# Optimization experiments

Hardware: AMD Instinct MI355X
Metric: run time of the kernel (lower is better)

Reference implementation:

```python
import jax, jax.numpy as jnp
import numpy as np

B = 16384
DIM_IN = 128; DIM_OUT = 128; DIM_X = 512; DIM_NL = 128
EPS = 1e-3; ALPHA = 1.0; STD = 0.5
DIM_H = 2 * DIM_X + DIM_NL


def setup_inputs() -> dict:
    key = jax.random.key(0)
    ks = jax.random.split(key, 8)
    u_in = jax.random.normal(ks[0], (B, 1, DIM_IN), jnp.float32)
    X = STD * jax.random.normal(ks[1], (DIM_H, DIM_H), jnp.float32)
    Y = STD * jax.random.normal(ks[2], (DIM_X, DIM_X), jnp.float32)
    B2 = STD * jax.random.normal(ks[3], (DIM_X, DIM_IN), jnp.float32)
    C2 = STD * jax.random.normal(ks[4], (DIM_OUT, DIM_X), jnp.float32)
    D21 = STD * jax.random.normal(ks[5], (DIM_OUT, DIM_NL), jnp.float32)
    D22 = STD * jax.random.normal(ks[6], (DIM_OUT, DIM_IN), jnp.float32)
    D12 = STD * jax.random.normal(ks[7], (DIM_NL, DIM_IN), jnp.float32)
    x0 = jnp.zeros((1, 1, DIM_X), jnp.float32)
    return {"u_in": u_in, "X": X, "Y": Y, "B2": B2, "C2": C2,
            "D21": D21, "D22": D22, "D12": D12, "x0": x0}


def reference(u_in, X, Y, B2, C2, D21, D22, D12, x0):
    # --- derived contractive parameterization (torch _update_model_param) ---
    H = X.T @ X + EPS * jnp.eye(DIM_H, dtype=X.dtype)
    H11 = H[:DIM_X, :DIM_X]
    H21 = H[DIM_X:DIM_X + DIM_NL, :DIM_X]
    H22 = H[DIM_X:DIM_X + DIM_NL, DIM_X:DIM_X + DIM_NL]
    H31 = H[DIM_X + DIM_NL:, :DIM_X]
    H32 = H[DIM_X + DIM_NL:, DIM_X:DIM_X + DIM_NL]
    H33 = H[DIM_X + DIM_NL:, DIM_X + DIM_NL:]
    F = H31                               # [X, X]
    B1 = H32                              # [X, NL]
    E = 0.5 * (H11 + ALPHA * H33 + Y - Y.T)  # [X, X]
    Lam = 0.5 * jnp.diagonal(H22)            # [NL]
    D11 = -jnp.tril(H22, k=-1)               # strictly lower triangular [NL, NL]
    C1 = -H21                                # [NL, X]

    u = u_in[:, 0, :]      # [B, in]
    x = x0[0, 0, :]        # [X], broadcast over batch as in torch
    xc = C1 @ x            # [NL] (x @ C1row^T per row, shared across batch)
    ud = u @ D12.T         # [B, NL] (precomputed; same math as per-row matmul)

    # sequential forward-substitution with tanh per row (strict lower tri D11)
    def step(w, inp):
        i, d11row, xci, lam = inp
        v = xci + ud[:, i] + w @ d11row        # [B]
        return w.at[:, i].set(jnp.tanh(v / lam)), None

    w0 = jnp.zeros((u.shape[0], DIM_NL), u.dtype)
    w, _ = jax.lax.scan(step, w0, (jnp.arange(DIM_NL), D11, xc, Lam))

    # state update: x+ = (x F^T + w B1^T + u B2^T) E^{-T}
    pre = (F @ x)[None, :] + w @ B1.T + u @ B2.T   # [B, X]
    x_new = pre @ jnp.linalg.inv(E).T              # [B, X]
    # output
    y = x_new @ C2.T + w @ D21.T + u @ D22.T       # [B, out]
    return y[:, None, :]
```

## Files before the change

### kernel.cpp

```cpp
#include <hip/hip_runtime.h>
#include <math.h>

#define EPS_C 0.001f
#define BATCH 16384

__global__ __launch_bounds__(256) void k_xtx(const float* __restrict__ X, float* __restrict__ H) {
  __shared__ float smem[64 * 65];
  const int bi64 = blockIdx.x, bj64 = blockIdx.y;
  if (bi64 > bj64) return;
  float (*sA)[65] = (float(*)[65])smem;
  float (*sB)[65] = (float(*)[65])(smem + 32 * 65);
  const int t = threadIdx.x;
  const int bi = bi64 * 64, bj = bj64 * 64;
  const int tj = t & 15, ti = t >> 4;
  float acc[4][4] = {};
  for (int k0 = 0; k0 < 1152; k0 += 32) {
    #pragma unroll
    for (int l = 0; l < 2; ++l) {
      int idx = t + l * 256;
      int kk = idx >> 4, c4 = (idx & 15) << 2;
      float4 va = *(const float4*)&X[(k0 + kk) * 1152 + bi + c4];
      sA[kk][c4 + 0] = va.x; sA[kk][c4 + 1] = va.y; sA[kk][c4 + 2] = va.z; sA[kk][c4 + 3] = va.w;
      float4 vb = *(const float4*)&X[(k0 + kk) * 1152 + bj + c4];
      sB[kk][c4 + 0] = vb.x; sB[kk][c4 + 1] = vb.y; sB[kk][c4 + 2] = vb.z; sB[kk][c4 + 3] = vb.w;
    }
    __syncthreads();
    #pragma unroll
    for (int kk = 0; kk < 32; ++kk) {
      float am[4], bn[4];
      #pragma unroll
      for (int q = 0; q < 4; ++q) am[q] = sA[kk][ti * 4 + q];
      #pragma unroll
      for (int q = 0; q < 4; ++q) bn[q] = sB[kk][tj * 4 + q];
      #pragma unroll
      for (int r = 0; r < 4; ++r)
        #pragma unroll
        for (int c = 0; c < 4; ++c)
          acc[r][c] = fmaf(am[r], bn[c], acc[r][c]);
    }
    __syncthreads();
  }
  #pragma unroll
  for (int r = 0; r < 4; ++r) {
    int gi = bi + ti * 4 + r;
    float vv[4];
    #pragma unroll
    for (int c = 0; c < 4; ++c) {
      vv[c] = acc[r][c];
      if (gi == bj + tj * 4 + c) vv[c] += EPS_C;
    }
    float4 o = make_float4(vv[0], vv[1], vv[2], vv[3]);
    *(float4*)&H[gi * 1152 + bj + tj * 4] = o;
  }
  if (bi64 < bj64) {
    float (*tr)[65] = (float(*)[65])smem;
    #pragma unroll
    for (int r = 0; r < 4; ++r)
      #pragma unroll
      for (int c = 0; c < 4; ++c)
        tr[tj * 4 + c][ti * 4 + r] = acc[r][c];
    __syncthreads();
    #pragma unroll
    for (int l = 0; l < 4; ++l) {
      int e = t + l * 256;
      int row = e >> 4, c4 = (e & 15) << 2;
      float4 o = make_float4(tr[row][c4], tr[row][c4 + 1], tr[row][c4 + 2], tr[row][c4 + 3]);
      *(float4*)&H[(bj + row) * 1152 + bi + c4] = o;
    }
  }
}

__global__ __launch_bounds__(256) void k_assemble(const float* __restrict__ H, const float* __restrict__ Y,
                           const float* __restrict__ C2, const float* __restrict__ x0,
                           float* __restrict__ M, float* __restrict__ D11,
                           float* __restrict__ Lam, float* __restrict__ xc, float* __restrict__ Fx) {
  const int b = blockIdx.x;
  const int t = threadIdx.x;
  if (b < 256) {
    __shared__ float tA[32][33], tB[32][33], tC[32][33];
    const int R0 = (b & 15) * 32, C0 = (b >> 4) * 32;
    const int c = t & 31, rr = t >> 5;
    #pragma unroll
    for (int p = 0; p < 4; ++p) {
      int row = rr + p * 8;
      tA[row][c] = H[(C0 + row) * 1152 + R0 + c];
      tB[row][c] = H[(640 + C0 + row) * 1152 + 640 + R0 + c];
      tC[row][c] = Y[(C0 + row) * 512 + R0 + c];
    }
    __syncthreads();
    #pragma unroll
    for (int p = 0; p < 4; ++p) {
      int r = rr + p * 8;
      float val = 0.5f * (tA[c][r] + tB[c][r] + tC[c][r] - Y[(R0 + r) * 512 + C0 + c]);
      M[(R0 + r) * 640 + C0 + c] = val;
    }
  } else if (b < 320) {
    int e0 = (b - 256) * 1024;
    #pragma unroll
    for (int l = 0; l < 4; ++l) {
      int e = e0 + l * 256 + t;
      int r = e >> 7, o = e & 127;
      M[r * 640 + 512 + o] = C2[o * 512 + r];
    }
  } else if (b < 384) {
    int e = (b - 320) * 256 + t;
    int i = e >> 7, j = e & 127;
    D11[e] = (j < i) ? -H[(512 + i) * 1152 + 512 + j] : 0.0f;
  } else if (b == 384) {
    if (t < 128) Lam[t] = 0.5f * H[(512 + t) * 1152 + 512 + t];
  } else if (b == 385) {
    if (t < 128) {
      float s = 0.f;
      for (int a = 0; a < 512; ++a) s = fmaf(H[(512 + t) * 1152 + a], x0[a], s);
      xc[t] = -s;
    }
  } else {
    int r = (b - 386) * 256 + t;
    float s = 0.f;
    for (int a = 0; a < 512; ++a) s = fmaf(H[(640 + r) * 1152 + a], x0[a], s);
    Fx[r] = s;
  }
}

__global__ __launch_bounds__(64) void k_lu_dp(float* __restrict__ M, float* __restrict__ Dfac, int kb) {
  __shared__ float sD[64 * 65];
  __shared__ float sRD[64];
  const int t = threadIdx.x;
  const int nU = 9 - kb;
  const int pb = blockIdx.x;
  float v[64];
  int c = 0, rr = 0;
  if (pb < nU) {
    c = 64 * (kb + 1) + pb * 64 + t;
    #pragma unroll
    for (int i = 0; i < 64; ++i) v[i] = M[(kb * 64 + i) * 640 + c];
  } else {
    rr = 64 * (kb + 1) + (pb - nU) * 64 + t;
    #pragma unroll
    for (int i = 0; i < 16; ++i) *(float4*)&v[i * 4] = *(const float4*)&M[rr * 640 + kb * 64 + i * 4];
  }
  {
    const float* blk = M + kb * 64 * 640 + kb * 64;
    float col[64];
    #pragma unroll
    for (int r = 0; r < 64; ++r) col[r] = blk[r * 640 + t];
    float invp = 1.0f;
    #pragma unroll
    for (int k = 0; k < 64; ++k) {
      float piv = __shfl(col[k], k);
      float inv = 1.0f / piv;
      if (t == k) invp = inv;
      float m = col[k] * inv;
      bool act = t > k;
      #pragma unroll
      for (int r = k + 1; r < 64; ++r) {
        float ckr = __shfl(col[r], k);
        if (act) col[r] -= ckr * m;
      }
    }
    #pragma unroll
    for (int r = 0; r < 64; ++r) {
      if (r > t) col[r] *= invp;
      sD[r * 65 + t] = col[r];
      if (pb == 0) Dfac[kb * 4096 + r * 64 + t] = col[r];
    }
    sRD[t] = invp;
  }
  __syncthreads();
  if (pb < nU) {
    #pragma unroll
    for (int i = 1; i < 64; ++i) {
      float a0 = v[i], a1 = 0.f;
      #pragma unroll
      for (int j = 0; j < i; j += 2) {
        a0 = fmaf(-sD[i * 65 + j], v[j], a0);
        if (j + 1 < i) a1 = fmaf(-sD[i * 65 + j + 1], v[j + 1], a1);
      }
      v[i] = a0 + a1;
    }
    #pragma unroll
    for (int i = 0; i < 64; ++i) M[(kb * 64 + i) * 640 + c] = v[i];
  } else {
    #pragma unroll
    for (int j = 0; j < 64; ++j) {
      float a0 = v[j], a1 = 0.f;
      #pragma unroll
      for (int i = 0; i < j; i += 2) {
        a0 = fmaf(-v[i], sD[i * 65 + j], a0);
        if (i + 1 < j) a1 = fmaf(-v[i + 1], sD[(i + 1) * 65 + j], a1);
      }
      v[j] = (a0 + a1) * sRD[j];
    }
    #pragma unroll
    for (int i = 0; i < 16; ++i) *(float4*)&M[rr * 640 + kb * 64 + i * 4] = *(float4*)&v[i * 4];
  }
}

__global__ __launch_bounds__(256) void k_lu_trailing(float* __restrict__ M, int kb) {
  __shared__ float sL[32][65];
  __shared__ float sU[32][65];
  const int t = threadIdx.x;
  const int base = 64 * (kb + 1);
  const int r0 = base + blockIdx.y * 64, c0 = base + blockIdx.x * 64;
  const int tj = t & 15, ti = t >> 4;
  float acc[4][4] = {};
  for (int k0 = 0; k0 < 64; k0 += 32) {
    #pragma unroll
    for (int l = 0; l < 2; ++l) {
      int idx = t + l * 256;
      int row = idx >> 3, k4 = (idx & 7) << 2;
      float4 v = *(const float4*)&M[(r0 + row) * 640 + kb * 64 + k0 + k4];
      sL[k4 + 0][row] = v.x; sL[k4 + 1][row] = v.y; sL[k4 + 2][row] = v.z; sL[k4 + 3][row] = v.w;
      int kk = idx >> 4, c4 = (idx & 15) << 2;
      float4 u4 = *(const float4*)&M[(kb * 64 + k0 + kk) * 640 + c0 + c4];
      sU[kk][c4 + 0] = u4.x; sU[kk][c4 + 1] = u4.y; sU[kk][c4 + 2] = u4.z; sU[kk][c4 + 3] = u4.w;
    }
    __syncthreads();
    #pragma unroll
    for (int kk = 0; kk < 32; ++kk) {
      float am[4], bn[4];
      #pragma unroll
      for (int q = 0; q < 4; ++q) am[q] = sL[kk][ti * 4 + q];
      #pragma unroll
      for (int q = 0; q < 4; ++q) bn[q] = sU[kk][tj * 4 + q];
      #pragma unroll
      for (int r = 0; r < 4; ++r)
        #pragma unroll
        for (int c = 0; c < 4; ++c)
          acc[r][c] = fmaf(am[r], bn[c], acc[r][c]);
    }
    __syncthreads();
  }
  #pragma unroll
  for (int r = 0; r < 4; ++r) {
    float4 old = *(float4*)&M[(r0 + ti * 4 + r) * 640 + c0 + tj * 4];
    old.x -= acc[r][0]; old.y -= acc[r][1]; old.z -= acc[r][2]; old.w -= acc[r][3];
    *(float4*)&M[(r0 + ti * 4 + r) * 640 + c0 + tj * 4] = old;
  }
}

__global__ __launch_bounds__(64) void k_inv(const float* __restrict__ Dfac, float* __restrict__ invU) {
  __shared__ float sD[64 * 65];
  __shared__ float srs[64];
  const int t = threadIdx.x;
  const int kb = blockIdx.x;
  for (int l = 0; l < 64; ++l) sD[l * 65 + t] = Dfac[kb * 4096 + l * 64 + t];
  __syncthreads();
  srs[t] = 1.0f / sD[t * 65 + t];
  __syncthreads();
  float v[64];
  #pragma unroll
  for (int i = 0; i < 64; ++i) v[i] = (i == t) ? srs[t] : 0.0f;
  #pragma unroll
  for (int i = 62; i >= 0; --i) {
    float a0 = 0.f, a1 = 0.f;
    #pragma unroll
    for (int j = i + 1; j < 64; j += 2) {
      a0 = fmaf(-sD[i * 65 + j], v[j], a0);
      if (j + 1 < 64) a1 = fmaf(-sD[i * 65 + j + 1], v[j + 1], a1);
    }
    float nv = (a0 + a1) * srs[i];
    v[i] = (i == t) ? v[i] : nv;
  }
  #pragma unroll
  for (int i = 0; i < 64; ++i) invU[kb * 4096 + i * 64 + t] = v[i];
}

__global__ __launch_bounds__(512, 2) void k_bs(const float* __restrict__ M, const float* __restrict__ invUg,
                                               float* __restrict__ Gt) {
  __shared__ float sZ[512 * 17];
  __shared__ float sU[64 * 65];
  __shared__ float sI[64 * 65];
  const int t = threadIdx.x;
  const int c0 = blockIdx.x * 16;
  const int o = t & 15, q = t >> 4;
  #pragma unroll
  for (int l = 0; l < 16; ++l) {
    int e = t + l * 512;
    int r = e >> 4, oo = e & 15;
    sZ[r * 17 + oo] = M[r * 640 + 512 + c0 + oo];
  }
  for (int kb = 7; kb >= 0; --kb) {
    #pragma unroll
    for (int l = 0; l < 8; ++l) {
      int e = t + l * 512;
      int r = e >> 6, k = e & 63;
      sI[r * 65 + k] = invUg[kb * 4096 + r * 64 + k];
    }
    __syncthreads();
    float xv[2];
    #pragma unroll
    for (int rr = 0; rr < 2; ++rr) {
      int i = q * 2 + rr;
      float a0 = 0.f, a1 = 0.f;
      #pragma unroll
      for (int k = 0; k < 64; k += 2) {
        a0 = fmaf(sI[i * 65 + k], sZ[(kb * 64 + k) * 17 + o], a0);
        a1 = fmaf(sI[i * 65 + k + 1], sZ[(kb * 64 + k + 1) * 17 + o], a1);
      }
      xv[rr] = a0 + a1;
    }
    __syncthreads();
    #pragma unroll
    for (int rr = 0; rr < 2; ++rr) {
      int i = q * 2 + rr;
      sZ[(kb * 64 + i) * 17 + o] = xv[rr];
      Gt[(kb * 64 + i) * 128 + c0 + o] = xv[rr];
    }
    __syncthreads();
    if (kb == 0) break;
    float xk[64];
    #pragma unroll
    for (int k = 0; k < 64; ++k) xk[k] = sZ[(kb * 64 + k) * 17 + o];
    float bufA[8], bufB[8];
    #pragma unroll
    for (int l = 0; l < 8; ++l) {
      int e = t + l * 512;
      int r = e >> 6, k = e & 63;
      bufA[l] = M[r * 640 + kb * 64 + k];
    }
    for (int i = 0; i < kb; ++i) {
      #pragma unroll
      for (int l = 0; l < 8; ++l) {
        int e = t + l * 512;
        int r = e >> 6, k = e & 63;
        sU[r * 65 + k] = bufA[l];
      }
      if (i + 1 < kb) {
        #pragma unroll
        for (int l = 0; l < 8; ++l) {
          int e = t + l * 512;
          int r = e >> 6, k = e & 63;
          bufB[l] = M[((i + 1) * 64 + r) * 640 + kb * 64 + k];
        }
      }
      __syncthreads();
      #pragma unroll
      for (int rr = 0; rr < 2; ++rr) {
        int row = q * 2 + rr;
        float acc = sZ[(i * 64 + row) * 17 + o];
        #pragma unroll
        for (int k = 0; k < 64; ++k)
          acc = fmaf(-sU[row * 65 + k], xk[k], acc);
        sZ[(i * 64 + row) * 17 + o] = acc;
      }
      #pragma unroll
      for (int l = 0; l < 8; ++l) bufA[l] = bufB[l];
      __syncthreads();
    }
  }
}

__global__ void k_wass(const float* __restrict__ Gt, const float* __restrict__ H,
                       const float* __restrict__ B2, const float* __restrict__ D21,
                       const float* __restrict__ D22, const float* __restrict__ Fx,
                       float* __restrict__ W1, float* __restrict__ W2, float* __restrict__ bias) {
  int idx = blockIdx.x * 256 + threadIdx.x;
  if (idx < 16384) {
    int o = idx >> 7, j = idx & 127;
    float s = 0.f;
    for (int a = 0; a < 512; ++a) s = fmaf(Gt[a * 128 + o], H[(640 + a) * 1152 + 512 + j], s);
    W1[idx] = s + D21[idx];
  } else if (idx < 32768) {
    int q = idx - 16384;
    int o = q >> 7, j = q & 127;
    float s = 0.f;
    for (int a = 0; a < 512; ++a) s = fmaf(Gt[a * 128 + o], B2[a * 128 + j], s);
    W2[q] = s + D22[q];
  } else if (idx < 32768 + 128) {
    int o = idx - 32768;
    float s = 0.f;
    for (int a = 0; a < 512; ++a) s = fmaf(Gt[a * 128 + o], Fx[a], s);
    bias[o] = s;
  }
}

__global__ __launch_bounds__(256) void k_ud(const float* __restrict__ u, const float* __restrict__ D12,
                                            const float* __restrict__ xc, float* __restrict__ baseT) {
  __shared__ float sU[32][65];
  __shared__ float sD[32][65];
  const int t = threadIdx.x;
  const int b0 = blockIdx.x * 64, i0 = blockIdx.y * 64;
  const int tm = t & 15, tn = t >> 4;
  float acc[4][4] = {};
  for (int k0 = 0; k0 < 128; k0 += 32) {
    #pragma unroll
    for (int l = 0; l < 2; ++l) {
      int idx = t + l * 256;
      int row = idx >> 3, k4 = (idx & 7) << 2;
      float4 v = *(const float4*)&u[(b0 + row) * 128 + k0 + k4];
      sU[k4 + 0][row] = v.x; sU[k4 + 1][row] = v.y; sU[k4 + 2][row] = v.z; sU[k4 + 3][row] = v.w;
      float4 d = *(const float4*)&D12[(i0 + row) * 128 + k0 + k4];
      sD[k4 + 0][row] = d.x; sD[k4 + 1][row] = d.y; sD[k4 + 2][row] = d.z; sD[k4 + 3][row] = d.w;
    }
    __syncthreads();
    #pragma unroll
    for (int kk = 0; kk < 32; ++kk) {
      float mm[4], nn[4];
      #pragma unroll
      for (int q = 0; q < 4; ++q) mm[q] = sU[kk][tm * 4 + q];
      #pragma unroll
      for (int q = 0; q < 4; ++q) nn[q] = sD[kk][tn * 4 + q];
      #pragma unroll
      for (int c = 0; c < 4; ++c)
        #pragma unroll
        for (int r = 0; r < 4; ++r)
          acc[c][r] = fmaf(nn[c], mm[r], acc[c][r]);
    }
    __syncthreads();
  }
  #pragma unroll
  for (int c = 0; c < 4; ++c) {
    int i = i0 + tn * 4 + c;
    float xcv = xc[i];
    float4 v = make_float4(acc[c][0] + xcv, acc[c][1] + xcv, acc[c][2] + xcv, acc[c][3] + xcv);
    *(float4*)&baseT[i * BATCH + b0 + tm * 4] = v;
  }
}

template<int I>
struct ScanStep {
  static __device__ __forceinline__ void run(float (&w)[128], const float* __restrict__ baseT,
                                             const float* __restrict__ D11g, const float* __restrict__ Lam,
                                             float* __restrict__ wT, int b) {
    ScanStep<I - 1>::run(w, baseT, D11g, Lam, wT, b);
    float acc0 = baseT[I * BATCH + b], acc1 = 0.f, acc2 = 0.f, acc3 = 0.f;
    const float* __restrict__ Drow = D11g + I * 128;
    #pragma unroll
    for (int j = 0; j + 4 <= I; j += 4) {
      acc0 = fmaf(w[j + 0], Drow[j + 0], acc0);
      acc1 = fmaf(w[j + 1], Drow[j + 1], acc1);
      acc2 = fmaf(w[j + 2], Drow[j + 2], acc2);
      acc3 = fmaf(w[j + 3], Drow[j + 3], acc3);
    }
    #pragma unroll
    for (int j = I & ~3; j < I; ++j) acc0 = fmaf(w[j], Drow[j], acc0);
    float zv = ((acc0 + acc1) + (acc2 + acc3)) / Lam[I];
    float az = fabsf(zv);
    float e = __expf(-2.0f * az);
    float th = (1.0f - e) / (1.0f + e);
    w[I] = copysignf(th, zv);
    wT[I * BATCH + b] = w[I];
  }
};
template<>
struct ScanStep<-1> {
  static __device__ __forceinline__ void run(float (&)[128], const float*, const float*, const float*,
                                             float*, int) {}
};

__global__ __launch_bounds__(64, 1) void k_scan(const float* __restrict__ baseT, const float* __restrict__ D11g,
                                                const float* __restrict__ Lam, float* __restrict__ wT) {
  const int b = blockIdx.x * 64 + threadIdx.x;
  float w[128];
  ScanStep<127>::run(w, baseT, D11g, Lam, wT, b);
}

__global__ __launch_bounds__(256) void k_y(const float* __restrict__ wT, const float* __restrict__ u,
                                           const float* __restrict__ W1, const float* __restrict__ W2,
                                           const float* __restrict__ bias, float* __restrict__ y) {
  __shared__ float sA[32][65];
  __shared__ float sW[32][65];
  const int t = threadIdx.x;
  const int b0 = blockIdx.x * 64, o0 = blockIdx.y * 64;
  const int tn = t & 15, tm = t >> 4;
  float acc[4][4] = {};
  for (int k0 = 0; k0 < 128; k0 += 32) {
    #pragma unroll
    for (int l = 0; l < 2; ++l) {
      int idx = t + l * 256;
      int kk = idx >> 4, c4 = (idx & 15) << 2;
      float4 v = *(const float4*)&wT[(k0 + kk) * BATCH + b0 + c4];
      sA[kk][c4 + 0] = v.x; sA[kk][c4 + 1] = v.y; sA[kk][c4 + 2] = v.z; sA[kk][c4 + 3] = v.w;
      int row = idx >> 3, k4 = (idx & 7) << 2;
      float4 d = *(const float4*)&W1[(o0 + row) * 128 + k0 + k4];
      sW[k4 + 0][row] = d.x; sW[k4 + 1][row] = d.y; sW[k4 + 2][row] = d.z; sW[k4 + 3][row] = d.w;
    }
    __syncthreads();
    #pragma unroll
    for (int kk = 0; kk < 32; ++kk) {
      float mm[4], nn[4];
      #pragma unroll
      for (int q = 0; q < 4; ++q) mm[q] = sA[kk][tm * 4 + q];
      #pragma unroll
      for (int q = 0; q < 4; ++q) nn[q] = sW[kk][tn * 4 + q];
      #pragma unroll
      for (int r = 0; r < 4; ++r)
        #pragma unroll
        for (int c = 0; c < 4; ++c)
          acc[r][c] = fmaf(mm[r], nn[c], acc[r][c]);
    }
    __syncthreads();
  }
  for (int k0 = 0; k0 < 128; k0 += 32) {
    #pragma unroll
    for (int l = 0; l < 2; ++l) {
      int idx = t + l * 256;
      int row = idx >> 3, k4 = (idx & 7) << 2;
      float4 v = *(const float4*)&u[(b0 + row) * 128 + k0 + k4];
      sA[k4 + 0][row] = v.x; sA[k4 + 1][row] = v.y; sA[k4 + 2][row] = v.z; sA[k4 + 3][row] = v.w;
      float4 d = *(const float4*)&W2[(o0 + row) * 128 + k0 + k4];
      sW[k4 + 0][row] = d.x; sW[k4 + 1][row] = d.y; sW[k4 + 2][row] = d.z; sW[k4 + 3][row] = d.w;
    }
    __syncthreads();
    #pragma unroll
    for (int kk = 0; kk < 32; ++kk) {
      float mm[4], nn[4];
      #pragma unroll
      for (int q = 0; q < 4; ++q) mm[q] = sA[kk][tm * 4 + q];
      #pragma unroll
      for (int q = 0; q < 4; ++q) nn[q] = sW[kk][tn * 4 + q];
      #pragma unroll
      for (int r = 0; r < 4; ++r)
        #pragma unroll
        for (int c = 0; c < 4; ++c)
          acc[r][c] = fmaf(mm[r], nn[c], acc[r][c]);
    }
    __syncthreads();
  }
  #pragma unroll
  for (int r = 0; r < 4; ++r) {
    int bb = b0 + tm * 4 + r;
    float4 v = make_float4(acc[r][0] + bias[o0 + tn * 4 + 0],
                           acc[r][1] + bias[o0 + tn * 4 + 1],
                           acc[r][2] + bias[o0 + tn * 4 + 2],
                           acc[r][3] + bias[o0 + tn * 4 + 3]);
    *(float4*)&y[bb * 128 + o0 + tn * 4] = v;
  }
}

extern "C" void kernel_launch(void* const* d_in, const int* in_sizes, int n_in,
                              void* d_out, int out_size, void* d_ws, size_t ws_size,
                              hipStream_t stream) {
  const float* u   = (const float*)d_in[0];
  const float* X   = (const float*)d_in[1];
  const float* Y   = (const float*)d_in[2];
  const float* B2  = (const float*)d_in[3];
  const float* C2  = (const float*)d_in[4];
  const float* D21 = (const float*)d_in[5];
  const float* D22 = (const float*)d_in[6];
  const float* D12 = (const float*)d_in[7];
  const float* x0  = (const float*)d_in[8];

  float* ws = (float*)d_ws;
  float* H     = ws;
  float* M     = H + 1327104;
  float* Gt    = M + 327680;
  float* W1    = Gt + 65536;
  float* W2    = W1 + 16384;
  float* D11   = W2 + 16384;
  float* Lam   = D11 + 16384;
  float* xc    = Lam + 128;
  float* Fx    = xc + 128;
  float* bias  = Fx + 512;
  float* baseT = bias + 128 + 64;
  float* wT    = baseT;
  float* Dfac  = H;
  float* invUg = H + 32768;
  float* y     = (float*)d_out;

  k_xtx<<<dim3(18, 18), 256, 0, stream>>>(X, H);
  k_assemble<<<388, 256, 0, stream>>>(H, Y, C2, x0, M, D11, Lam, xc, Fx);

  for (int kb = 0; kb < 8; ++kb) {
    k_lu_dp<<<16 - 2 * kb, 64, 0, stream>>>(M, Dfac, kb);
    if (kb < 7)
      k_lu_trailing<<<dim3(9 - kb, 7 - kb), 256, 0, stream>>>(M, kb);
  }

  k_inv<<<8, 64, 0, stream>>>(Dfac, invUg);
  k_bs<<<8, 512, 0, stream>>>(M, invUg, Gt);
  k_wass<<<129, 256, 0, stream>>>(Gt, H, B2, D21, D22, Fx, W1, W2, bias);

  k_ud<<<dim3(256, 2), 256, 0, stream>>>(u, D12, xc, baseT);
  k_scan<<<256, 64, 0, stream>>>(baseT, D11, Lam, wT);
  k_y<<<dim3(256, 2), 256, 0, stream>>>(wT, u, W1, W2, bias, y);
}
```

Measured before the change: 912.5 us.

## Block the tanh scan into 16-wide chunks with LDS-resident history

Replaces the fully unrolled 128-register scan with a chunked loop. Each chunk of 16 outputs is held in registers, and earlier outputs are read back from LDS as float4 vectors. This lowers register pressure and code size and drops the one-wave-per-SIMD launch bound, so more waves can hide latency. The cost is extra LDS traffic and a runtime loop over earlier chunks instead of fully unrolled register FMAs.

Result: slower. 950.4 us (+4.1%).

```diff
diff --git a/kernel.cpp b/kernel.cpp
--- a/kernel.cpp
+++ b/kernel.cpp
@@ -418,42 +418,48 @@
   }
 }
 
-template<int I>
-struct ScanStep {
-  static __device__ __forceinline__ void run(float (&w)[128], const float* __restrict__ baseT,
-                                             const float* __restrict__ D11g, const float* __restrict__ Lam,
-                                             float* __restrict__ wT, int b) {
-    ScanStep<I - 1>::run(w, baseT, D11g, Lam, wT, b);
-    float acc0 = baseT[I * BATCH + b], acc1 = 0.f, acc2 = 0.f, acc3 = 0.f;
-    const float* __restrict__ Drow = D11g + I * 128;
-    #pragma unroll
-    for (int j = 0; j + 4 <= I; j += 4) {
-      acc0 = fmaf(w[j + 0], Drow[j + 0], acc0);
-      acc1 = fmaf(w[j + 1], Drow[j + 1], acc1);
-      acc2 = fmaf(w[j + 2], Drow[j + 2], acc2);
-      acc3 = fmaf(w[j + 3], Drow[j + 3], acc3);
-    }
-    #pragma unroll
-    for (int j = I & ~3; j < I; ++j) acc0 = fmaf(w[j], Drow[j], acc0);
-    float zv = ((acc0 + acc1) + (acc2 + acc3)) / Lam[I];
-    float az = fabsf(zv);
-    float e = __expf(-2.0f * az);
-    float th = (1.0f - e) / (1.0f + e);
-    w[I] = copysignf(th, zv);
-    wT[I * BATCH + b] = w[I];
-  }
-};
-template<>
-struct ScanStep<-1> {
-  static __device__ __forceinline__ void run(float (&)[128], const float*, const float*, const float*,
-                                             float*, int) {}
-};
-
-__global__ __launch_bounds__(64, 1) void k_scan(const float* __restrict__ baseT, const float* __restrict__ D11g,
-                                                const float* __restrict__ Lam, float* __restrict__ wT) {
-  const int b = blockIdx.x * 64 + threadIdx.x;
-  float w[128];
-  ScanStep<127>::run(w, baseT, D11g, Lam, wT, b);
+__global__ __launch_bounds__(64) void k_scan(const float* __restrict__ baseT, const float* __restrict__ D11g,
+                                             const float* __restrict__ Lam, float* __restrict__ wT) {
+  __shared__ float wl[32 * 260];
+  const int t = threadIdx.x;
+  const int b = blockIdx.x * 64 + t;
+  for (int c = 0; c < 8; ++c) {
+    const int C = c * 16;
+    float bt[16];
+    #pragma unroll
+    for (int l = 0; l < 16; ++l) bt[l] = baseT[(C + l) * BATCH + b];
+    float wc[16];
+    #pragma unroll
+    for (int li = 0; li < 16; ++li) {
+      const int i = C + li;
+      float acc0 = bt[li], acc1 = 0.f, acc2 = 0.f, acc3 = 0.f;
+      const float* __restrict__ Drow = D11g + i * 128;
+      for (int g = 0; g < C / 4; ++g) {
+        float4 wv = *(const float4*)&wl[g * 260 + t * 4];
+        acc0 = fmaf(wv.x, Drow[g * 4 + 0], acc0);
+        acc1 = fmaf(wv.y, Drow[g * 4 + 1], acc1);
+        acc2 = fmaf(wv.z, Drow[g * 4 + 2], acc2);
+        acc3 = fmaf(wv.w, Drow[g * 4 + 3], acc3);
+      }
+      #pragma unroll
+      for (int lg = 0; lg + 4 <= li; lg += 4) {
+        acc0 = fmaf(wc[lg + 0], Drow[C + lg + 0], acc0);
+        acc1 = fmaf(wc[lg + 1], Drow[C + lg + 1], acc1);
+        acc2 = fmaf(wc[lg + 2], Drow[C + lg + 2], acc2);
+        acc3 = fmaf(wc[lg + 3], Drow[C + lg + 3], acc3);
+      }
+      #pragma unroll
+      for (int lj = li & ~3; lj < li; ++lj) acc0 = fmaf(wc[lj], Drow[C + lj], acc0);
+      float zv = ((acc0 + acc1) + (acc2 + acc3)) / Lam[i];
+      float az = fabsf(zv);
+      float e = __expf(-2.0f * az);
+      float th = (1.0f - e) / (1.0f + e);
+      float wi = copysignf(th, zv);
+      wc[li] = wi;
+      wl[(i >> 2) * 260 + t * 4 + (i & 3)] = wi;
+      wT[i * BATCH + b] = wi;
+    }
+  }
 }
 
 __global__ __launch_bounds__(256) void k_y(const float* __restrict__ wT, const float* __restrict__ u,
```
